# Performance work log

Measured on AMD Instinct MI355X. Metric: run time of the kernel, lower is better.

## Reference

```python
import jax, jax.numpy as jnp
from jax import lax
import numpy as np
import math

B, L, D = 2, 1536, 1024
H = 8
C = 2 * D          # d_wide
DPH = C // H       # 256, dim_per_head
K = 4              # causal conv kernel size


def _ln(x, w, b=None, eps=1e-5):
    mu = jnp.mean(x, -1, keepdims=True)
    var = jnp.mean((x - mu) ** 2, -1, keepdims=True)
    y = (x - mu) * lax.rsqrt(var + eps) * w
    return y + b if b is not None else y


def setup_inputs() -> dict:
    key = jax.random.key(0)
    ks = jax.random.split(key, 8)
    x = jax.random.normal(ks[0], (B, L, D), jnp.float32)
    ln_w = jnp.ones((D,), jnp.float32)
    ln_b = jnp.zeros((D,), jnp.float32)
    w1 = jax.random.normal(ks[1], (4 * D, D), jnp.float32) * math.sqrt(2.0 / 5.0 / D)
    b1 = jnp.zeros((4 * D,), jnp.float32)
    conv_w = jax.random.normal(ks[2], (C, C, K), jnp.float32) * (1.0 / math.sqrt(C * K))
    conv_b = jnp.zeros((C,), jnp.float32)
    skip = jnp.ones((C,), jnp.float32)
    wqk = jax.random.normal(ks[3], (H, DPH, 2 * DPH), jnp.float32) * (1.0 / math.sqrt(DPH))
    bqk = jnp.zeros((H, 2 * DPH), jnp.float32)
    wv = jax.random.normal(ks[4], (H, DPH, DPH), jnp.float32) * (1.0 / math.sqrt(DPH))
    bv = jnp.zeros((H, DPH), jnp.float32)
    wif = jnp.zeros((2 * H, 3 * C), jnp.float32)  # zero-init per source
    bif = jnp.concatenate([jax.random.normal(ks[5], (H,), jnp.float32) * 0.1,
                           jnp.linspace(3.0, 6.0, H, dtype=jnp.float32)])
    hn_w = jnp.ones((DPH,), jnp.float32)
    w2 = jax.random.normal(ks[6], (D, C), jnp.float32) * (2.0 / 24.0 / math.sqrt(D))
    b2 = jnp.zeros((D,), jnp.float32)
    return {"x": x, "ln_w": ln_w, "ln_b": ln_b, "w1": w1, "b1": b1,
            "conv_w": conv_w, "conv_b": conv_b, "skip": skip,
            "wqk": wqk, "bqk": bqk, "wv": wv, "bv": bv,
            "wif": wif, "bif": bif, "hn_w": hn_w, "w2": w2, "b2": b2}


def _causal_conv(x1, conv_w, conv_b):
    # literal translation: permute(1,2,0), left-pad last dim, conv1d, permute(2,0,1)
    t = jnp.transpose(x1, (1, 2, 0))                  # (L, C, B)
    t = jnp.pad(t, ((0, 0), (0, 0), (K - 1, 0)))      # left pad along dim0 of original
    o = lax.conv_general_dilated(t, conv_w, (1,), 'VALID',
                                 dimension_numbers=('NCH', 'OIH', 'NCH'))
    o = o + conv_b[None, :, None]
    return jnp.transpose(o, (2, 0, 1))                # (B, L, C)


def _mlstm_core(qk, v_in, wqk, bqk, wv, bv, wif, bif, hn_w):
    b_, l_, c_ = qk.shape
    qkh = qk.reshape(b_, l_, H, DPH)
    proj = jnp.einsum('blhi,hio->blho', qkh, wqk) + bqk       # (B,L,H,2*DPH)
    q, k = jnp.split(proj, 2, axis=-1)                        # each (B,L,H,DPH)
    v = jnp.einsum('blhi,hio->blho', v_in.reshape(b_, l_, H, DPH), wv) + bv
    qkv = jnp.concatenate([proj, v], axis=-1).reshape(b_, l_, 3 * c_)
    gates = qkv @ wif.T + bif                                 # (B,L,2H)
    i_g, f_g = jnp.split(gates, 2, axis=-1)                   # (B,L,H)
    i_g = jnp.exp(i_g)
    f_c = jnp.cumsum(jax.nn.log_sigmoid(f_g), axis=1)
    fmat = f_c[:, :, None, :] - f_c[:, None, :, :]            # (B,o,i,H)
    mask = jnp.triu(jnp.ones((l_, l_), bool), 1)[None, :, :, None]
    fmat = jnp.where(mask, -jnp.inf, fmat)
    d = fmat + i_g[:, None, :, :]
    m = jnp.max(d, axis=-2, keepdims=True)                    # over i: (B,o,1,H)
    d = jnp.exp(d - m)
    ks_ = k / math.sqrt(DPH)
    c = jnp.einsum('bohd,bihd->boih', q, ks_) * d
    bsum = jnp.sum(c, axis=-2, keepdims=True)                 # (B,o,1,H)
    n = jnp.maximum(jnp.abs(bsum), jnp.exp(-m))
    c = c / n
    h = jnp.einsum('boih,bihd->bohd', c, v)                   # (B,L,H,DPH)
    h = _ln(h, hn_w)                                          # LayerNorm, no bias
    return h.reshape(b_, l_, c_)


def reference(x, ln_w, ln_b, w1, b1, conv_w, conv_b, skip, wqk, bqk, wv, bv,
              wif, bif, hn_w, w2, b2):
    y = _ln(x, ln_w, ln_b) @ w1.T + b1                        # (B,L,4D)
    x1, x2 = jnp.split(y, 2, axis=-1)                         # each (B,L,C)
    qk = jax.nn.silu(_causal_conv(x1, conv_w, conv_b))
    h = _mlstm_core(qk, x1, wqk, bqk, wv, bv, wif, bif, hn_w)
    x1o = h + skip * qk
    xm = x1o * jax.nn.silu(x2)
    return xm @ w2.T + b2 + x
```

## Files before the change

kernel.cpp:

```cpp
#include <hip/hip_runtime.h>

typedef unsigned short u16;
typedef __bf16 bf16x8 __attribute__((ext_vector_type(8)));
typedef float f32x4 __attribute__((ext_vector_type(4)));
typedef unsigned short us8 __attribute__((ext_vector_type(8)));

#define MFMA(a,b,c) __builtin_amdgcn_mfma_f32_16x16x32_bf16((a),(b),(c),0,0,0)
#define DEV __device__ __forceinline__

DEV u16 f2bf(float f){
  unsigned u = __float_as_uint(f);
  u += 0x7fffu + ((u >> 16) & 1u);
  return (u16)(u >> 16);
}
DEV float silu_f(float v){ return v / (1.f + __expf(-v)); }
DEV bf16x8 asbf(us8 v){ return __builtin_bit_cast(bf16x8, v); }
DEV void gl16(const u16* g, u16* l){
  __builtin_amdgcn_global_load_lds((const __attribute__((address_space(1))) void*)g,
                                   (__attribute__((address_space(3))) void*)l, 16, 0, 0);
}

__global__ void prep_kernel(const float* __restrict__ w1, const float* __restrict__ w2,
                            const float* __restrict__ wif, const float* __restrict__ conv_w,
                            const float* __restrict__ wqk, const float* __restrict__ wv,
                            u16* __restrict__ w1b, u16* __restrict__ w2b, u16* __restrict__ wifb,
                            u16* __restrict__ cw2, u16* __restrict__ cw3,
                            u16* __restrict__ wqkt, u16* __restrict__ wvt)
{
  const long N0 = 4194304;
  const long N1 = N0 + 2097152;
  const long N2 = N1 + 98304;
  const long N3 = N2 + 4194304;
  const long N4 = N3 + 4194304;
  const long N5 = N4 + 1048576;
  const long N6 = N5 + 524288;
  long stride = (long)gridDim.x * blockDim.x;
  for (long i = (long)blockIdx.x*blockDim.x + threadIdx.x; i < N6; i += stride) {
    if (i < N0)      { w1b[i] = f2bf(w1[i]); }
    else if (i < N1) { long j = i-N0; w2b[j] = f2bf(w2[j]); }
    else if (i < N2) { long j = i-N1; wifb[j] = f2bf(wif[j]); }
    else if (i < N3) { long j = i-N2; cw2[j] = f2bf(conv_w[j*4+2]); }
    else if (i < N4) { long j = i-N3; cw3[j] = f2bf(conv_w[j*4+3]); }
    else if (i < N5) { long j = i-N4; long h=j>>17, r=j&131071, o=r>>8, ii=r&255;
                       wqkt[j] = f2bf(wqk[h*131072 + ii*512 + o]); }
    else             { long j = i-N5; long h=j>>16, o=(j>>8)&255, ii=j&255;
                       wvt[j] = f2bf(wv[h*65536 + ii*256 + o]); }
  }
}

__global__ __launch_bounds__(256) void ln_kernel(const float* __restrict__ x,
        const float* __restrict__ w, const float* __restrict__ b, u16* __restrict__ xn)
{
  int row = blockIdx.x, tid = threadIdx.x;
  const float* xr = x + (long)row*1024;
  float4 v = *(const float4*)(xr + tid*4);
  float s = v.x+v.y+v.z+v.w;
  float q = v.x*v.x+v.y*v.y+v.z*v.z+v.w*v.w;
  #pragma unroll
  for (int off=32; off>=1; off>>=1){ s += __shfl_xor(s,off); q += __shfl_xor(q,off); }
  __shared__ float red[8];
  int wv_ = tid>>6;
  if ((tid&63)==0){ red[wv_*2]=s; red[wv_*2+1]=q; }
  __syncthreads();
  s = red[0]+red[2]+red[4]+red[6];
  q = red[1]+red[3]+red[5]+red[7];
  float mu = s*(1.f/1024.f);
  float var = q*(1.f/1024.f) - mu*mu;
  float rs = rsqrtf(var + 1e-5f);
  int c = tid*4;
  u16 o0 = f2bf((v.x-mu)*rs*w[c+0] + b[c+0]);
  u16 o1 = f2bf((v.y-mu)*rs*w[c+1] + b[c+1]);
  u16 o2 = f2bf((v.z-mu)*rs*w[c+2] + b[c+2]);
  u16 o3 = f2bf((v.w-mu)*rs*w[c+3] + b[c+3]);
  uint2 pk;
  pk.x = (unsigned)o0 | ((unsigned)o1<<16);
  pk.y = (unsigned)o2 | ((unsigned)o3<<16);
  *(uint2*)(xn + (long)row*1024 + c) = pk;
}

__global__ __launch_bounds__(256,2) void gemm_bt(
    const u16* __restrict__ A, long lda, long sAz,
    const u16* __restrict__ A2,
    const u16* __restrict__ Bm, long ldb, long sBz,
    const u16* __restrict__ B2,
    int K1, int Ktot,
    const float* __restrict__ bias, long sBiasz,
    int epi,
    float* __restrict__ outf, long ldo,
    u16* __restrict__ outb, long ldob, long sObz,
    const float* __restrict__ resid,
    float* __restrict__ outf2)
{
  __shared__ u16 AsF[4096];
  __shared__ u16 BsF[4096];
  int tid = threadIdx.x;
  int bz = blockIdx.z;
  A += (long)bz*sAz; Bm += (long)bz*sBz;
  const float* biasz = bias ? (bias + (long)bz*sBiasz) : bias;
  u16* outbz = outb ? (outb + (long)bz*sObz) : outb;
  long am0 = (long)blockIdx.y*128;
  long bn0 = (long)blockIdx.x*128;
  int lane = tid&63, wave = tid>>6, quad = lane>>4, l15 = lane&15;
  int wm = wave>>1, wn = wave&1;
  int kq8 = quad*8;
  f32x4 acc[4][4] = {};
  for (int k0=0; k0<Ktot; k0+=32) {
    const u16* Ak = A; const u16* Bk = Bm; int kk = k0;
    if (k0 >= K1){ Ak = A2; Bk = B2; kk = k0 - K1; }
    __syncthreads();
    gl16(Ak + (am0 + wave*16 + l15)*lda + kk + kq8,       AsF + wave*512);
    gl16(Ak + (am0 + (wave+4)*16 + l15)*lda + kk + kq8,   AsF + (wave+4)*512);
    gl16(Bk + (bn0 + wave*16 + l15)*ldb + kk + kq8,       BsF + wave*512);
    gl16(Bk + (bn0 + (wave+4)*16 + l15)*ldb + kk + kq8,   BsF + (wave+4)*512);
    __syncthreads();
    bf16x8 af[4], bfr[4];
    #pragma unroll
    for (int t=0;t<4;t++){
      af[t]  = *(const bf16x8*)&AsF[(wm*4+t)*512 + quad*128 + l15*8];
      bfr[t] = *(const bf16x8*)&BsF[(wn*4+t)*512 + quad*128 + l15*8];
    }
    #pragma unroll
    for (int ti=0;ti<4;ti++)
      #pragma unroll
      for (int tj=0;tj<4;tj++)
        acc[ti][tj] = MFMA(af[ti], bfr[tj], acc[ti][tj]);
  }
  #pragma unroll
  for (int ti=0;ti<4;ti++)
  #pragma unroll
  for (int tj=0;tj<4;tj++)
  #pragma unroll
  for (int r=0;r<4;r++){
    long m = am0 + wm*64 + ti*16 + quad*4 + r;
    long n = bn0 + wn*64 + tj*16 + l15;
    float v = acc[ti][tj][r];
    if (epi==1){ outbz[m*ldob+n] = f2bf(v + biasz[n]); }
    else if (epi==2){
      v += biasz[n];
      if (n < 2048) outbz[m*ldob+n] = f2bf(v);
      else outf2[m*2048 + n - 2048] = silu_f(v);
    }
    else if (epi==3){
      v += biasz[n]; v = silu_f(v);
      outf[m*ldo+n] = v; outbz[m*ldob+n] = f2bf(v);
    }
    else { outf[m*ldo+n] = v + biasz[n] + resid[m*1024+n]; }
  }
}

__global__ __launch_bounds__(256) void gates_gemm(const u16* __restrict__ qkv,
        const u16* __restrict__ wifb, float* __restrict__ gates)
{
  int tid = threadIdx.x;
  int lane = tid&63, wave = tid>>6, quad = lane>>4, l15 = lane&15;
  long m0 = (long)blockIdx.x*128 + wave*32;
  int ks = blockIdx.y*1536;
  const u16* arow = qkv + (m0 + l15)*6144;
  const u16* brow = wifb + (long)l15*6144;
  f32x4 acc[2] = {};
  for (int k0=ks; k0<ks+1536; k0+=32){
    bf16x8 a0 = *(const bf16x8*)(arow + k0 + quad*8);
    bf16x8 a1 = *(const bf16x8*)(arow + (long)16*6144 + k0 + quad*8);
    bf16x8 bb = *(const bf16x8*)(brow + k0 + quad*8);
    acc[0] = MFMA(a0,bb,acc[0]);
    acc[1] = MFMA(a1,bb,acc[1]);
  }
  #pragma unroll
  for (int mt=0;mt<2;mt++)
  #pragma unroll
  for (int r=0;r<4;r++)
    atomicAdd(&gates[(m0 + mt*16 + quad*4 + r)*16 + l15], acc[mt][r]);
}

__global__ void scan_kernel(const float* __restrict__ gates, const float* __restrict__ bif,
        float* __restrict__ g_arr, float* __restrict__ mg_arr, float* __restrict__ enm)
{
  int bh = blockIdx.x; int b = bh>>3, h = bh&7;
  int lane = threadIdx.x;
  float bi = bif[h], bff = bif[8+h];
  float fl[24], gl[24];
  int l0 = lane*24;
  float s = 0.f;
  #pragma unroll
  for (int j=0;j<24;j++){
    int l = l0+j;
    float f = gates[((long)(b*1536+l))*16 + 8 + h] + bff;
    float ls = fminf(f,0.f) - log1pf(expf(-fabsf(f)));
    fl[j] = ls; s += ls;
  }
  float tot = s;
  for (int off=1; off<64; off<<=1){ float t = __shfl_up(s, off); if (lane>=off) s += t; }
  float fc = s - tot;
  float lm = -INFINITY;
  #pragma unroll
  for (int j=0;j<24;j++){
    int l = l0+j;
    fc += fl[j];
    fl[j] = fc;
    float ir = gates[((long)(b*1536+l))*16 + h] + bi;
    float g = expf(ir) - fc;
    gl[j] = g;
    lm = fmaxf(lm, g);
  }
  float im = lm;
  for (int off=1; off<64; off<<=1){ float t = __shfl_up(im, off); if (lane>=off) im = fmaxf(im,t); }
  float ex = __shfl_up(im, 1);
  if (lane==0) ex = -INFINITY;
  float rm = ex;
  #pragma unroll
  for (int j=0;j<24;j++){
    rm = fmaxf(rm, gl[j]);
    long idx = (long)bh*1536 + l0 + j;
    g_arr[idx] = gl[j];
    mg_arr[idx] = rm;
    enm[idx] = expf(-(fl[j] + rm));
  }
}

__global__ __launch_bounds__(256) void vtrans_kernel(const u16* __restrict__ qkv, u16* __restrict__ vtg)
{
  int l = blockIdx.x*256 + threadIdx.x;
  int bh = blockIdx.y; int b = bh>>3, h = bh&7;
  const u16* src = qkv + ((long)(b*1536+l))*6144 + h*768 + 512;
  u16* dst = vtg + (long)bh*256*1536 + l;
  #pragma unroll
  for (int c=0;c<32;c++){
    us8 v = *(const us8*)(src + c*8);
    #pragma unroll
    for (int j=0;j<8;j++) dst[(long)(c*8+j)*1536] = v[j];
  }
}

__global__ __launch_bounds__(256,2) void attn_kernel(
    const u16* __restrict__ qkv, const u16* __restrict__ vtg,
    const float* __restrict__ g_arr, const float* __restrict__ mg_arr,
    const float* __restrict__ enm,
    const float* __restrict__ hn_w, const float* __restrict__ skip,
    const float* __restrict__ qkf, const float* __restrict__ s2,
    u16* __restrict__ xm)
{
  __shared__ u16 pl[4][32][40];
  __shared__ float red[256*36];
  __shared__ float redb[3][32];
  int tid = threadIdx.x;
  int lane = tid&63, wave = tid>>6, quad = lane>>4, l15 = lane&15;
  int bh = blockIdx.x, b = bh>>3, h = bh&7;
  int otile = 47 - blockIdx.y;
  int ow0 = otile*32;
  us8 qreg[2][8];
  #pragma unroll
  for (int mt=0;mt<2;mt++)
    #pragma unroll
    for (int kc=0;kc<8;kc++)
      qreg[mt][kc] = *(const us8*)(qkv + ((long)(b*1536 + ow0 + mt*16 + l15))*6144 + h*768 + kc*32 + quad*8);
  float mg[2][4];
  #pragma unroll
  for (int mt=0;mt<2;mt++)
    #pragma unroll
    for (int r=0;r<4;r++)
      mg[mt][r] = mg_arr[(long)bh*1536 + ow0 + mt*16 + quad*4 + r];
  f32x4 accv[2][16] = {};
  float bs[2][4] = {};
  for (int it=wave; it<=otile; it+=4){
    int i0 = it*32;
    const u16* kbase = qkv + ((long)(b*1536 + i0))*6144 + h*768 + 256;
    f32x4 sacc[2][2] = {};
    #pragma unroll
    for (int kc=0;kc<8;kc++){
      bf16x8 b0 = *(const bf16x8*)(kbase + (long)l15*6144 + kc*32 + quad*8);
      bf16x8 b1 = *(const bf16x8*)(kbase + (long)(16+l15)*6144 + kc*32 + quad*8);
      sacc[0][0] = MFMA(asbf(qreg[0][kc]), b0, sacc[0][0]);
      sacc[0][1] = MFMA(asbf(qreg[0][kc]), b1, sacc[0][1]);
      sacc[1][0] = MFMA(asbf(qreg[1][kc]), b0, sacc[1][0]);
      sacc[1][1] = MFMA(asbf(qreg[1][kc]), b1, sacc[1][1]);
    }
    #pragma unroll
    for (int nt=0;nt<2;nt++){
      float gi = g_arr[(long)bh*1536 + i0 + nt*16 + l15];
      #pragma unroll
      for (int mt=0;mt<2;mt++)
        #pragma unroll
        for (int r=0;r<4;r++){
          int oi = ow0 + mt*16 + quad*4 + r;
          int ii = i0 + nt*16 + l15;
          float sv = sacc[mt][nt][r]*0.0625f;
          float p = (ii <= oi) ? sv*__expf(gi - mg[mt][r]) : 0.f;
          bs[mt][r] += p;
          pl[wave][mt*16+quad*4+r][nt*16+l15] = f2bf(p);
        }
    }
    bf16x8 pa0 = *(const bf16x8*)&pl[wave][l15][quad*8];
    bf16x8 pa1 = *(const bf16x8*)&pl[wave][16+l15][quad*8];
    #pragma unroll
    for (int tj=0;tj<16;tj++){
      bf16x8 vb = *(const bf16x8*)(vtg + ((long)(bh*256 + tj*16 + l15))*1536 + i0 + quad*8);
      accv[0][tj] = MFMA(pa0, vb, accv[0][tj]);
      accv[1][tj] = MFMA(pa1, vb, accv[1][tj]);
    }
  }
  #pragma unroll
  for (int mt=0;mt<2;mt++)
    #pragma unroll
    for (int r=0;r<4;r++)
      #pragma unroll
      for (int off=1; off<16; off<<=1) bs[mt][r] += __shfl_xor(bs[mt][r], off);
  for (int w=1; w<4; w++){
    if (wave==w){
      #pragma unroll
      for (int mt=0;mt<2;mt++)
        #pragma unroll
        for (int tj=0;tj<16;tj++)
          *(f32x4*)&red[(tj*16+l15)*36 + mt*16 + quad*4] = accv[mt][tj];
      if (l15==0){
        #pragma unroll
        for (int mt=0;mt<2;mt++)
          #pragma unroll
          for (int r=0;r<4;r++)
            redb[w-1][mt*16+quad*4+r] = bs[mt][r];
      }
    }
    __syncthreads();
    if (wave==0){
      #pragma unroll
      for (int mt=0;mt<2;mt++)
        #pragma unroll
        for (int tj=0;tj<16;tj++)
          accv[mt][tj] += *(const f32x4*)&red[(tj*16+l15)*36 + mt*16 + quad*4];
      #pragma unroll
      for (int mt=0;mt<2;mt++)
        #pragma unroll
        for (int r=0;r<4;r++)
          bs[mt][r] += redb[w-1][mt*16+quad*4+r];
    }
    __syncthreads();
  }
  if (wave != 0) return;
  long browg = (long)b*1536;
  #pragma unroll
  for (int mt=0;mt<2;mt++){
    #pragma unroll
    for (int r=0;r<4;r++){
      int row = ow0 + mt*16 + quad*4 + r;
      float s1 = 0.f, sq = 0.f;
      #pragma unroll
      for (int tj=0;tj<16;tj++){ float a = accv[mt][tj][r]; s1 += a; sq += a*a; }
      #pragma unroll
      for (int off=1; off<16; off<<=1){ s1 += __shfl_xor(s1,off); sq += __shfl_xor(sq,off); }
      float nv = fmaxf(fabsf(bs[mt][r]), enm[(long)bh*1536 + row]);
      float inv = 1.f/nv;
      float mu = s1*inv*(1.f/256.f);
      float var = sq*inv*inv*(1.f/256.f) - mu*mu;
      float rs = rsqrtf(var + 1e-5f);
      long rg = browg + row;
      #pragma unroll
      for (int tj=0;tj<16;tj++){
        int col = tj*16 + l15;
        int cc = h*256 + col;
        float y = (accv[mt][tj][r]*inv - mu)*rs*hn_w[col];
        float xv = (y + skip[cc]*qkf[rg*2048 + cc]) * s2[rg*2048 + cc];
        xm[rg*2048 + cc] = f2bf(xv);
      }
    }
  }
}

extern "C" void kernel_launch(void* const* d_in, const int* in_sizes, int n_in,
                              void* d_out, int out_size, void* d_ws, size_t ws_size,
                              hipStream_t stream)
{
  const float* x      = (const float*)d_in[0];
  const float* ln_w   = (const float*)d_in[1];
  const float* ln_b   = (const float*)d_in[2];
  const float* w1     = (const float*)d_in[3];
  const float* b1     = (const float*)d_in[4];
  const float* conv_w = (const float*)d_in[5];
  const float* conv_b = (const float*)d_in[6];
  const float* skip   = (const float*)d_in[7];
  const float* wqk    = (const float*)d_in[8];
  const float* bqk    = (const float*)d_in[9];
  const float* wv     = (const float*)d_in[10];
  const float* bv     = (const float*)d_in[11];
  const float* wif    = (const float*)d_in[12];
  const float* bif    = (const float*)d_in[13];
  const float* hn_w   = (const float*)d_in[14];
  const float* w2     = (const float*)d_in[15];
  const float* b2     = (const float*)d_in[16];
  float* out = (float*)d_out;

  char* p = (char*)d_ws;
  auto alloc = [&](size_t bytes)->void*{ void* r = (void*)p; p += (bytes + 255) & ~(size_t)255; return r; };
  u16* w1b  = (u16*)alloc((size_t)4194304*2);
  u16* w2b  = (u16*)alloc((size_t)2097152*2);
  u16* wifb = (u16*)alloc((size_t)98304*2);
  u16* cw2  = (u16*)alloc((size_t)4194304*2);
  u16* cw3  = (u16*)alloc((size_t)4194304*2);
  u16* wqkt = (u16*)alloc((size_t)1048576*2);
  u16* wvt  = (u16*)alloc((size_t)524288*2);
  u16* xn   = (u16*)alloc((size_t)3072*1024*2);
  u16* x1b  = (u16*)alloc((size_t)3072*2048*2);
  float* s2 = (float*)alloc((size_t)3072*2048*4);
  float* qkf= (float*)alloc((size_t)3072*2048*4);
  u16* qkb  = (u16*)alloc((size_t)3072*2048*2);
  u16* qkv  = (u16*)alloc((size_t)3072*6144*2);
  u16* vtg  = (u16*)alloc((size_t)16*256*1536*2);
  float* gates = (float*)alloc((size_t)3072*16*4);
  float* g_arr = (float*)alloc((size_t)16*1536*4);
  float* mg_arr= (float*)alloc((size_t)16*1536*4);
  float* enm   = (float*)alloc((size_t)16*1536*4);
  u16* xmb  = (u16*)alloc((size_t)3072*2048*2);
  if ((size_t)(p - (char*)d_ws) > ws_size) return;

  hipMemsetAsync(gates, 0, (size_t)3072*16*4, stream);
  prep_kernel<<<4096, 256, 0, stream>>>(w1, w2, wif, conv_w, wqk, wv,
                                        w1b, w2b, wifb, cw2, cw3, wqkt, wvt);
  ln_kernel<<<3072, 256, 0, stream>>>(x, ln_w, ln_b, xn);
  gemm_bt<<<dim3(32,24,1), 256, 0, stream>>>(xn, 1024, 0, nullptr, w1b, 1024, 0, nullptr,
       1024, 1024, b1, 0, 2, nullptr, 0, x1b, 2048, 0, nullptr, s2);
  gemm_bt<<<dim3(16,12,1), 256, 0, stream>>>(x1b, 2048, 0, nullptr, cw3, 2048, 0, nullptr,
       2048, 2048, conv_b, 0, 3, qkf, 2048, qkb, 2048, 0, nullptr, nullptr);
  gemm_bt<<<dim3(16,12,1), 256, 0, stream>>>(x1b, 2048, 0, x1b + (long)1536*2048,
       cw2, 2048, 0, cw3, 2048, 4096, conv_b, 0, 3,
       qkf + (long)1536*2048, 2048, qkb + (long)1536*2048, 2048, 0, nullptr, nullptr);
  gemm_bt<<<dim3(4,24,8), 256, 0, stream>>>(qkb, 2048, 256, nullptr, wqkt, 256, 131072, nullptr,
       256, 256, bqk, 512, 1, nullptr, 0, qkv, 6144, 768, nullptr, nullptr);
  gemm_bt<<<dim3(2,24,8), 256, 0, stream>>>(x1b, 2048, 256, nullptr, wvt, 256, 65536, nullptr,
       256, 256, bv, 256, 1, nullptr, 0, qkv + 512, 6144, 768, nullptr, nullptr);
  vtrans_kernel<<<dim3(6,16,1), 256, 0, stream>>>(qkv, vtg);
  gates_gemm<<<dim3(24,4,1), 256, 0, stream>>>(qkv, wifb, gates);
  scan_kernel<<<16, 64, 0, stream>>>(gates, bif, g_arr, mg_arr, enm);
  attn_kernel<<<dim3(16,48,1), 256, 0, stream>>>(qkv, vtg, g_arr, mg_arr, enm,
       hn_w, skip, qkf, s2, xmb);
  gemm_bt<<<dim3(8,24,1), 256, 0, stream>>>(xmb, 2048, 0, nullptr, w2b, 2048, 0, nullptr,
       2048, 2048, b2, 0, 4, out, 1024, nullptr, 0, 0, x, nullptr);
}
```

Before: 780.9 us.

## Repack Q/K/V into MFMA fragment tiles and merge conv GEMMs into one launch

Replaces the V transpose kernel with a repack kernel that writes Q, pre-scaled K and V into per-tile, fragment-ordered buffers. The attention kernel can then read them with contiguous per-lane loads instead of strided rows of the wide qkv tensor. The two conv GEMM launches are merged into one grid using blockIdx.z to pick single or dual K-range mode, and the prep kernel reads both conv taps with a single float2 load. The cost is an extra pass writing three repacked buffers, plus K being rounded to bf16 after the 1/16 scale.

```diff
diff --git a/kernel.cpp b/kernel.cpp
--- a/kernel.cpp
+++ b/kernel.cpp
@@ -13,12 +13,9 @@
   u += 0x7fffu + ((u >> 16) & 1u);
   return (u16)(u >> 16);
 }
+DEV float bf2f(u16 v){ return __uint_as_float(((unsigned)v)<<16); }
 DEV float silu_f(float v){ return v / (1.f + __expf(-v)); }
 DEV bf16x8 asbf(us8 v){ return __builtin_bit_cast(bf16x8, v); }
-DEV void gl16(const u16* g, u16* l){
-  __builtin_amdgcn_global_load_lds((const __attribute__((address_space(1))) void*)g,
-                                   (__attribute__((address_space(3))) void*)l, 16, 0, 0);
-}
 
 __global__ void prep_kernel(const float* __restrict__ w1, const float* __restrict__ w2,
                             const float* __restrict__ wif, const float* __restrict__ conv_w,
@@ -31,19 +28,18 @@
   const long N1 = N0 + 2097152;
   const long N2 = N1 + 98304;
   const long N3 = N2 + 4194304;
-  const long N4 = N3 + 4194304;
-  const long N5 = N4 + 1048576;
-  const long N6 = N5 + 524288;
+  const long N4 = N3 + 1048576;
+  const long N5 = N4 + 524288;
   long stride = (long)gridDim.x * blockDim.x;
-  for (long i = (long)blockIdx.x*blockDim.x + threadIdx.x; i < N6; i += stride) {
+  for (long i = (long)blockIdx.x*blockDim.x + threadIdx.x; i < N5; i += stride) {
     if (i < N0)      { w1b[i] = f2bf(w1[i]); }
     else if (i < N1) { long j = i-N0; w2b[j] = f2bf(w2[j]); }
     else if (i < N2) { long j = i-N1; wifb[j] = f2bf(wif[j]); }
-    else if (i < N3) { long j = i-N2; cw2[j] = f2bf(conv_w[j*4+2]); }
-    else if (i < N4) { long j = i-N3; cw3[j] = f2bf(conv_w[j*4+3]); }
-    else if (i < N5) { long j = i-N4; long h=j>>17, r=j&131071, o=r>>8, ii=r&255;
+    else if (i < N3) { long j = i-N2; float2 t = *(const float2*)(conv_w + j*4 + 2);
+                       cw2[j] = f2bf(t.x); cw3[j] = f2bf(t.y); }
+    else if (i < N4) { long j = i-N3; long h=j>>17, r=j&131071, o=r>>8, ii=r&255;
                        wqkt[j] = f2bf(wqk[h*131072 + ii*512 + o]); }
-    else             { long j = i-N5; long h=j>>16, o=(j>>8)&255, ii=j&255;
+    else             { long j = i-N4; long h=j>>16, o=(j>>8)&255, ii=j&255;
                        wvt[j] = f2bf(wv[h*65536 + ii*256 + o]); }
   }
 }
@@ -83,10 +79,10 @@
     const u16* __restrict__ A2,
     const u16* __restrict__ Bm, long ldb, long sBz,
     const u16* __restrict__ B2,
-    int K1, int Ktot,
+    int K1, int Ktot, int convmode,
     const float* __restrict__ bias, long sBiasz,
     int epi,
-    float* __restrict__ outf, long ldo,
+    float* __restrict__ outf, long ldo, long sOfz,
     u16* __restrict__ outb, long ldob, long sObz,
     const float* __restrict__ resid,
     float* __restrict__ outf2)
@@ -98,20 +94,30 @@
   A += (long)bz*sAz; Bm += (long)bz*sBz;
   const float* biasz = bias ? (bias + (long)bz*sBiasz) : bias;
   u16* outbz = outb ? (outb + (long)bz*sObz) : outb;
+  float* outfz = outf ? (outf + (long)bz*sOfz) : outf;
   long am0 = (long)blockIdx.y*128;
   long bn0 = (long)blockIdx.x*128;
   int lane = tid&63, wave = tid>>6, quad = lane>>4, l15 = lane&15;
   int wm = wave>>1, wn = wave&1;
   int kq8 = quad*8;
+  int dual = convmode && (bz==1);
+  int Kt = dual ? Ktot : K1;
   f32x4 acc[4][4] = {};
-  for (int k0=0; k0<Ktot; k0+=32) {
-    const u16* Ak = A; const u16* Bk = Bm; int kk = k0;
-    if (k0 >= K1){ Ak = A2; Bk = B2; kk = k0 - K1; }
+  for (int k0=0; k0<Kt; k0+=32) {
+    const u16* Ak; const u16* Bk; int kk;
+    if (dual){
+      if (k0 < K1){ Ak = A; Bk = B2; kk = k0; }
+      else        { Ak = A2; Bk = Bm; kk = k0 - K1; }
+    } else { Ak = A; Bk = Bm; kk = k0; }
     __syncthreads();
-    gl16(Ak + (am0 + wave*16 + l15)*lda + kk + kq8,       AsF + wave*512);
-    gl16(Ak + (am0 + (wave+4)*16 + l15)*lda + kk + kq8,   AsF + (wave+4)*512);
-    gl16(Bk + (bn0 + wave*16 + l15)*ldb + kk + kq8,       BsF + wave*512);
-    gl16(Bk + (bn0 + (wave+4)*16 + l15)*ldb + kk + kq8,   BsF + (wave+4)*512);
+    __builtin_amdgcn_global_load_lds((const __attribute__((address_space(1))) void*)(Ak + (am0 + wave*16 + l15)*lda + kk + kq8),
+                                     (__attribute__((address_space(3))) void*)(AsF + wave*512), 16, 0, 0);
+    __builtin_amdgcn_global_load_lds((const __attribute__((address_space(1))) void*)(Ak + (am0 + (wave+4)*16 + l15)*lda + kk + kq8),
+                                     (__attribute__((address_space(3))) void*)(AsF + (wave+4)*512), 16, 0, 0);
+    __builtin_amdgcn_global_load_lds((const __attribute__((address_space(1))) void*)(Bk + (bn0 + wave*16 + l15)*ldb + kk + kq8),
+                                     (__attribute__((address_space(3))) void*)(BsF + wave*512), 16, 0, 0);
+    __builtin_amdgcn_global_load_lds((const __attribute__((address_space(1))) void*)(Bk + (bn0 + (wave+4)*16 + l15)*ldb + kk + kq8),
+                                     (__attribute__((address_space(3))) void*)(BsF + (wave+4)*512), 16, 0, 0);
     __syncthreads();
     bf16x8 af[4], bfr[4];
     #pragma unroll
@@ -142,9 +148,9 @@
     }
     else if (epi==3){
       v += biasz[n]; v = silu_f(v);
-      outf[m*ldo+n] = v; outbz[m*ldob+n] = f2bf(v);
-    }
-    else { outf[m*ldo+n] = v + biasz[n] + resid[m*1024+n]; }
+      outfz[m*ldo+n] = v; outbz[m*ldob+n] = f2bf(v);
+    }
+    else { outfz[m*ldo+n] = v + biasz[n] + resid[m*1024+n]; }
   }
 }
 
@@ -217,22 +223,37 @@
   }
 }
 
-__global__ __launch_bounds__(256) void vtrans_kernel(const u16* __restrict__ qkv, u16* __restrict__ vtg)
-{
-  int l = blockIdx.x*256 + threadIdx.x;
-  int bh = blockIdx.y; int b = bh>>3, h = bh&7;
-  const u16* src = qkv + ((long)(b*1536+l))*6144 + h*768 + 512;
-  u16* dst = vtg + (long)bh*256*1536 + l;
-  #pragma unroll
-  for (int c=0;c<32;c++){
-    us8 v = *(const us8*)(src + c*8);
-    #pragma unroll
-    for (int j=0;j<8;j++) dst[(long)(c*8+j)*1536] = v[j];
+__global__ __launch_bounds__(256) void repack_kernel(const u16* __restrict__ qkv,
+        u16* __restrict__ qf, u16* __restrict__ kf, u16* __restrict__ vf)
+{
+  int bh = blockIdx.x, c = blockIdx.y;
+  int b = bh>>3, h = bh&7;
+  int tid = threadIdx.x;
+  long rowb = (long)b*1536 + c*32;
+  #pragma unroll
+  for (int s4=0; s4<4; s4++){
+    int s = s4*256 + tid;
+    int n16 = s>>9, kc=(s>>6)&7, l=s&63, quad=l>>4, l15=l&15;
+    const u16* src = qkv + (rowb + n16*16 + l15)*6144 + h*768 + kc*32 + quad*8;
+    us8 q = *(const us8*)src;
+    us8 k = *(const us8*)(src + 256);
+    us8 ksc;
+    #pragma unroll
+    for (int j=0;j<8;j++) ksc[j] = f2bf(bf2f(k[j])*0.0625f);
+    int tj = s>>6;
+    us8 v;
+    #pragma unroll
+    for (int j=0;j<8;j++)
+      v[j] = qkv[(rowb + quad*8 + j)*6144 + h*768 + 512 + tj*16 + l15];
+    long dst = ((long)(bh*48+c))*8192 + (long)s*8;
+    *(us8*)(qf+dst) = q;
+    *(us8*)(kf+dst) = ksc;
+    *(us8*)(vf+dst) = v;
   }
 }
 
 __global__ __launch_bounds__(256,2) void attn_kernel(
-    const u16* __restrict__ qkv, const u16* __restrict__ vtg,
+    const u16* __restrict__ qf, const u16* __restrict__ kf, const u16* __restrict__ vf,
     const float* __restrict__ g_arr, const float* __restrict__ mg_arr,
     const float* __restrict__ enm,
     const float* __restrict__ hn_w, const float* __restrict__ skip,
@@ -247,12 +268,13 @@
   int bh = blockIdx.x, b = bh>>3, h = bh&7;
   int otile = 47 - blockIdx.y;
   int ow0 = otile*32;
+  const u16* qfb = qf + ((long)(bh*48+otile))*8192;
   us8 qreg[2][8];
   #pragma unroll
   for (int mt=0;mt<2;mt++)
     #pragma unroll
     for (int kc=0;kc<8;kc++)
-      qreg[mt][kc] = *(const us8*)(qkv + ((long)(b*1536 + ow0 + mt*16 + l15))*6144 + h*768 + kc*32 + quad*8);
+      qreg[mt][kc] = *(const us8*)(qfb + mt*4096 + kc*512 + lane*8);
   float mg[2][4];
   #pragma unroll
   for (int mt=0;mt<2;mt++)
@@ -263,12 +285,12 @@
   float bs[2][4] = {};
   for (int it=wave; it<=otile; it+=4){
     int i0 = it*32;
-    const u16* kbase = qkv + ((long)(b*1536 + i0))*6144 + h*768 + 256;
+    const u16* kfb = kf + ((long)(bh*48+it))*8192;
     f32x4 sacc[2][2] = {};
     #pragma unroll
     for (int kc=0;kc<8;kc++){
-      bf16x8 b0 = *(const bf16x8*)(kbase + (long)l15*6144 + kc*32 + quad*8);
-      bf16x8 b1 = *(const bf16x8*)(kbase + (long)(16+l15)*6144 + kc*32 + quad*8);
+      bf16x8 b0 = *(const bf16x8*)(kfb + kc*512 + lane*8);
+      bf16x8 b1 = *(const bf16x8*)(kfb + 4096 + kc*512 + lane*8);
       sacc[0][0] = MFMA(asbf(qreg[0][kc]), b0, sacc[0][0]);
       sacc[0][1] = MFMA(asbf(qreg[0][kc]), b1, sacc[0][1]);
       sacc[1][0] = MFMA(asbf(qreg[1][kc]), b0, sacc[1][0]);
@@ -283,17 +305,17 @@
         for (int r=0;r<4;r++){
           int oi = ow0 + mt*16 + quad*4 + r;
           int ii = i0 + nt*16 + l15;
-          float sv = sacc[mt][nt][r]*0.0625f;
-          float p = (ii <= oi) ? sv*__expf(gi - mg[mt][r]) : 0.f;
+          float p = (ii <= oi) ? sacc[mt][nt][r]*__expf(gi - mg[mt][r]) : 0.f;
           bs[mt][r] += p;
           pl[wave][mt*16+quad*4+r][nt*16+l15] = f2bf(p);
         }
     }
+    const u16* vfb = vf + ((long)(bh*48+it))*8192;
     bf16x8 pa0 = *(const bf16x8*)&pl[wave][l15][quad*8];
     bf16x8 pa1 = *(const bf16x8*)&pl[wave][16+l15][quad*8];
     #pragma unroll
     for (int tj=0;tj<16;tj++){
-      bf16x8 vb = *(const bf16x8*)(vtg + ((long)(bh*256 + tj*16 + l15))*1536 + i0 + quad*8);
+      bf16x8 vb = *(const bf16x8*)(vfb + tj*512 + lane*8);
       accv[0][tj] = MFMA(pa0, vb, accv[0][tj]);
       accv[1][tj] = MFMA(pa1, vb, accv[1][tj]);
     }
@@ -402,7 +424,9 @@
   float* qkf= (float*)alloc((size_t)3072*2048*4);
   u16* qkb  = (u16*)alloc((size_t)3072*2048*2);
   u16* qkv  = (u16*)alloc((size_t)3072*6144*2);
-  u16* vtg  = (u16*)alloc((size_t)16*256*1536*2);
+  u16* qfb  = (u16*)alloc((size_t)16*48*8192*2);
+  u16* kfb  = (u16*)alloc((size_t)16*48*8192*2);
+  u16* vfb  = (u16*)alloc((size_t)16*48*8192*2);
   float* gates = (float*)alloc((size_t)3072*16*4);
   float* g_arr = (float*)alloc((size_t)16*1536*4);
   float* mg_arr= (float*)alloc((size_t)16*1536*4);
@@ -415,21 +439,19 @@
                                         w1b, w2b, wifb, cw2, cw3, wqkt, wvt);
   ln_kernel<<<3072, 256, 0, stream>>>(x, ln_w, ln_b, xn);
   gemm_bt<<<dim3(32,24,1), 256, 0, stream>>>(xn, 1024, 0, nullptr, w1b, 1024, 0, nullptr,
-       1024, 1024, b1, 0, 2, nullptr, 0, x1b, 2048, 0, nullptr, s2);
-  gemm_bt<<<dim3(16,12,1), 256, 0, stream>>>(x1b, 2048, 0, nullptr, cw3, 2048, 0, nullptr,
-       2048, 2048, conv_b, 0, 3, qkf, 2048, qkb, 2048, 0, nullptr, nullptr);
-  gemm_bt<<<dim3(16,12,1), 256, 0, stream>>>(x1b, 2048, 0, x1b + (long)1536*2048,
-       cw2, 2048, 0, cw3, 2048, 4096, conv_b, 0, 3,
-       qkf + (long)1536*2048, 2048, qkb + (long)1536*2048, 2048, 0, nullptr, nullptr);
+       1024, 1024, 0, b1, 0, 2, nullptr, 0, 0, x1b, 2048, 0, nullptr, s2);
+  gemm_bt<<<dim3(16,12,2), 256, 0, stream>>>(x1b, 2048, 0, x1b + (long)1536*2048,
+       cw3, 2048, 0, cw2, 2048, 4096, 1, conv_b, 0, 3,
+       qkf, 2048, (long)1536*2048, qkb, 2048, (long)1536*2048, nullptr, nullptr);
   gemm_bt<<<dim3(4,24,8), 256, 0, stream>>>(qkb, 2048, 256, nullptr, wqkt, 256, 131072, nullptr,
-       256, 256, bqk, 512, 1, nullptr, 0, qkv, 6144, 768, nullptr, nullptr);
+       256, 256, 0, bqk, 512, 1, nullptr, 0, 0, qkv, 6144, 768, nullptr, nullptr);
   gemm_bt<<<dim3(2,24,8), 256, 0, stream>>>(x1b, 2048, 256, nullptr, wvt, 256, 65536, nullptr,
-       256, 256, bv, 256, 1, nullptr, 0, qkv + 512, 6144, 768, nullptr, nullptr);
-  vtrans_kernel<<<dim3(6,16,1), 256, 0, stream>>>(qkv, vtg);
+       256, 256, 0, bv, 256, 1, nullptr, 0, 0, qkv + 512, 6144, 768, nullptr, nullptr);
+  repack_kernel<<<dim3(16,48,1), 256, 0, stream>>>(qkv, qfb, kfb, vfb);
   gates_gemm<<<dim3(24,4,1), 256, 0, stream>>>(qkv, wifb, gates);
   scan_kernel<<<16, 64, 0, stream>>>(gates, bif, g_arr, mg_arr, enm);
-  attn_kernel<<<dim3(16,48,1), 256, 0, stream>>>(qkv, vtg, g_arr, mg_arr, enm,
+  attn_kernel<<<dim3(16,48,1), 256, 0, stream>>>(qfb, kfb, vfb, g_arr, mg_arr, enm,
        hn_w, skip, qkf, s2, xmb);
   gemm_bt<<<dim3(8,24,1), 256, 0, stream>>>(xmb, 2048, 0, nullptr, w2b, 2048, 0, nullptr,
-       2048, 2048, b2, 0, 4, out, 1024, nullptr, 0, 0, x, nullptr);
-}
+       2048, 2048, 0, b2, 0, 4, out, 1024, 0, nullptr, 0, 0, x, nullptr);
+}
```

Result: faster. 653.1 us (-16.4%).
